# Kernel optimization log

Hardware: AMD Instinct MI355X
Metric: run time of the kernel (lower is better)

The kernel has to match this reference:

```python
import jax, jax.numpy as jnp
import numpy as np

B, S, DIM, H = 2, 2048, 2048, 16
HD = DIM // H  # 128
ROPE_THETA = 10000.0
NEG = -1e9


def setup_inputs() -> dict:
    key = jax.random.key(0)
    ks = jax.random.split(key, 6)
    x = jax.random.normal(ks[0], (B, S, DIM), dtype=jnp.float32)
    # rotary embedding tables: angle[s, j] = s / theta^(2j/HD), j in [0, HD/2)
    inv_freq = 1.0 / (ROPE_THETA ** (jnp.arange(0, HD, 2, dtype=jnp.float32) / HD))
    angles = jnp.arange(S, dtype=jnp.float32)[:, None] * inv_freq[None, :]  # (S, HD/2)
    freqs_cos = jnp.cos(angles)
    freqs_sin = jnp.sin(angles)
    # causal additive mask (1,1,S,S)
    causal = jnp.tril(jnp.ones((S, S), dtype=jnp.bool_))
    mask = jnp.where(causal, 0.0, NEG).astype(jnp.float32)[None, None]
    sc = 1.0 / np.sqrt(DIM)
    wq = jax.random.normal(ks[1], (DIM, DIM), dtype=jnp.float32) * sc
    wk = jax.random.normal(ks[2], (DIM, DIM), dtype=jnp.float32) * sc
    wv = jax.random.normal(ks[3], (DIM, DIM), dtype=jnp.float32) * sc
    wo = jax.random.normal(ks[4], (DIM, DIM), dtype=jnp.float32) * sc
    return {"x": x, "freqs_cos": freqs_cos, "freqs_sin": freqs_sin,
            "mask": mask, "wq": wq, "wk": wk, "wv": wv, "wo": wo}


def _apply_rope(t, cos, sin):
    # t: (B,S,H,HD); cos/sin: (S, HD/2) -> broadcast (1,S,1,HD/2)
    tr = t[..., ::2]
    ti = t[..., 1::2]
    c = cos[None, :, None, :]
    s = sin[None, :, None, :]
    out_r = tr * c - ti * s
    out_i = tr * s + ti * c
    # interleave back: stack on last axis then flatten -> [r0,i0,r1,i1,...]
    return jnp.stack([out_r, out_i], axis=-1).reshape(t.shape)


def reference(x, freqs_cos, freqs_sin, mask, wq, wk, wv, wo):
    b, s, _ = x.shape
    xq = (x @ wq).reshape(b, s, H, HD)
    xk = (x @ wk).reshape(b, s, H, HD)
    xv = (x @ wv).reshape(b, s, H, HD)
    xq = _apply_rope(xq, freqs_cos, freqs_sin)
    xk = _apply_rope(xk, freqs_cos, freqs_sin)
    # (B,H,S,HD)
    q = jnp.transpose(xq, (0, 2, 1, 3)) * (1.0 / np.sqrt(HD))
    k = jnp.transpose(xk, (0, 2, 1, 3))
    v = jnp.transpose(xv, (0, 2, 1, 3))
    attn = jnp.einsum('bhqd,bhkd->bhqk', q, k) + mask[:, :, :s, :s]
    attn = jax.nn.softmax(attn, axis=-1)
    out = jnp.einsum('bhqk,bhkd->bhqd', attn, v)  # (B,H,S,HD)
    out = jnp.transpose(out, (0, 2, 1, 3)).reshape(b, s, H * HD)
    return out @ wo
```

## Files before the change

### kernel.cpp

```cpp
#include <hip/hip_runtime.h>
#include <hip/hip_bf16.h>
#include <cstdint>
#include <cstddef>

#define BB   2
#define SS   2048
#define DD   2048
#define HH   16
#define HDD  128

typedef unsigned short u16;
typedef __attribute__((ext_vector_type(8))) short short8;
typedef __attribute__((ext_vector_type(4))) float f32x4;

__device__ __forceinline__ u16 f2bf(float f) {
  union { float f; uint32_t u; } v; v.f = f;
  uint32_t r = v.u + 0x7fffu + ((v.u >> 16) & 1u);
  return (u16)(r >> 16);
}
__device__ __forceinline__ float bf2f(u16 b) {
  union { uint32_t u; float f; } v; v.u = ((uint32_t)b) << 16;
  return v.f;
}

__device__ __forceinline__ void gload16(const u16* g, u16* l) {
  __builtin_amdgcn_global_load_lds(
      (__attribute__((address_space(1))) void*)g,
      (__attribute__((address_space(3))) void*)l, 16, 0, 0);
}

__global__ void k_cvt(const float* __restrict__ x, u16* __restrict__ o) {
  int i = blockIdx.x * blockDim.x + threadIdx.x;
  const float4 v = reinterpret_cast<const float4*>(x)[i];
  uint2 p;
  p.x = (uint32_t)f2bf(v.x) | ((uint32_t)f2bf(v.y) << 16);
  p.y = (uint32_t)f2bf(v.z) | ((uint32_t)f2bf(v.w) << 16);
  reinterpret_cast<uint2*>(o)[i] = p;
}

__global__ void k_wt(const float* __restrict__ w, u16* __restrict__ wt) {
  __shared__ float t[32][33];
  const int n0 = blockIdx.x * 32, k0 = blockIdx.y * 32;
  const int tx = threadIdx.x, ty = threadIdx.y;
#pragma unroll
  for (int i = 0; i < 32; i += 8)
    t[ty + i][tx] = w[(size_t)(k0 + ty + i) * DD + n0 + tx];
  __syncthreads();
#pragma unroll
  for (int i = 0; i < 32; i += 8)
    wt[(size_t)(n0 + ty + i) * DD + k0 + tx] = f2bf(t[tx][ty + i]);
}

__global__ void k_vt(const u16* __restrict__ V, u16* __restrict__ Vt) {
  __shared__ u16 t[32][33];
  const int s0 = blockIdx.x * 32, d0 = blockIdx.y * 32, bh = blockIdx.z;
  const u16* vb = V + (size_t)bh * SS * HDD;
  u16* vt = Vt + (size_t)bh * SS * HDD;
  const int tx = threadIdx.x, ty = threadIdx.y;
#pragma unroll
  for (int i = 0; i < 32; i += 8)
    t[ty + i][tx] = vb[(size_t)(s0 + ty + i) * HDD + d0 + tx];
  __syncthreads();
#pragma unroll
  for (int i = 0; i < 32; i += 8)
    vt[(size_t)(d0 + ty + i) * SS + s0 + tx] = t[tx][ty + i];
}

__global__ void k_rope(u16* __restrict__ Q, u16* __restrict__ Kb,
                       const float* __restrict__ fc, const float* __restrict__ fs) {
  const int idx = blockIdx.x * blockDim.x + threadIdx.x;
  const int p = idx & 63;
  const int s = (idx >> 6) & (SS - 1);
  const float cv = fc[s * 64 + p], sv = fs[s * 64 + p];
  const size_t off = ((size_t)(idx >> 6)) * HDD + p * 2;
  const float sc = 0.08838834764831845f;
  const float qr = bf2f(Q[off]), qi = bf2f(Q[off + 1]);
  Q[off]      = f2bf((qr * cv - qi * sv) * sc);
  Q[off + 1]  = f2bf((qr * sv + qi * cv) * sc);
  const float kr = bf2f(Kb[off]), ki = bf2f(Kb[off + 1]);
  Kb[off]     = f2bf(kr * cv - ki * sv);
  Kb[off + 1] = f2bf(kr * sv + ki * cv);
}

template <int MODE>
__global__ __launch_bounds__(256) void k_gemm(const u16* __restrict__ A,
                                              const u16* __restrict__ Bt,
                                              void* __restrict__ out) {
  __shared__ __align__(16) u16 As[128 * 32];
  __shared__ __align__(16) u16 Bs[128 * 32];
  const int tid = threadIdx.x;
  const int wave = tid >> 6, lane = tid & 63;
  const int c = lane & 15, g = lane >> 4;
  const int row0 = blockIdx.x * 128, col0 = blockIdx.y * 128;
  const int wm = wave >> 1, wn = wave & 1;
  const int sr = lane >> 2;
  const int sk = (lane & 3) * 8;
  f32x4 acc[4][4] = {};
  for (int k0 = 0; k0 < DD; k0 += 32) {
#pragma unroll
    for (int r = 0; r < 2; ++r) {
      const int chunk = r * 4 + wave;
      const int row = chunk * 16 + sr;
      gload16(A  + (size_t)(row0 + row) * DD + k0 + sk, As + chunk * 512);
      gload16(Bt + (size_t)(col0 + row) * DD + k0 + sk, Bs + chunk * 512);
    }
    __syncthreads();
    short8 a[4], b[4];
#pragma unroll
    for (int i = 0; i < 4; ++i)
      a[i] = *reinterpret_cast<const short8*>(As + (wm * 64 + i * 16 + c) * 32 + g * 8);
#pragma unroll
    for (int j = 0; j < 4; ++j)
      b[j] = *reinterpret_cast<const short8*>(Bs + (wn * 64 + j * 16 + c) * 32 + g * 8);
#pragma unroll
    for (int i = 0; i < 4; ++i)
#pragma unroll
      for (int j = 0; j < 4; ++j)
        acc[i][j] = __builtin_amdgcn_mfma_f32_16x16x32_bf16(a[i], b[j], acc[i][j], 0, 0, 0);
    __syncthreads();
  }
#pragma unroll
  for (int i = 0; i < 4; ++i) {
#pragma unroll
    for (int j = 0; j < 4; ++j) {
      const int mb = row0 + wm * 64 + i * 16 + g * 4;
      const int n  = col0 + wn * 64 + j * 16 + c;
#pragma unroll
      for (int r = 0; r < 4; ++r) {
        const int m = mb + r;
        if (MODE == 0) {
          const int b_ = m >> 11, s_ = m & (SS - 1);
          const int h_ = n >> 7,  d_ = n & (HDD - 1);
          reinterpret_cast<u16*>(out)[(((size_t)(b_ * HH + h_)) * SS + s_) * HDD + d_] =
              f2bf(acc[i][j][r]);
        } else {
          reinterpret_cast<float*>(out)[(size_t)m * DD + n] = acc[i][j][r];
        }
      }
    }
  }
}

__global__ __launch_bounds__(256, 3) void k_attn(const u16* __restrict__ Q,
                                                 const u16* __restrict__ K,
                                                 const u16* __restrict__ Vt,
                                                 u16* __restrict__ O) {
  __shared__ __align__(16) u16 Kt[64 * 128];
  __shared__ __align__(16) u16 Vs[128 * 64];
  __shared__ __align__(16) u16 Pb[4 * 32 * 72];
  const int tid = threadIdx.x;
  const int wave = tid >> 6, lane = tid & 63;
  const int c = lane & 15, g = lane >> 4;
  const int l = blockIdx.x;
  int qi, bh;
  if (l < 256) { qi = 8 + (l & 7); bh = l >> 3; }
  else         { qi = 7 - ((l - 256) & 7); bh = (l - 256) >> 3; }
  const int q0 = qi * 128;
  const u16* Qp = Q  + (size_t)bh * SS * HDD;
  const u16* Kp = K  + (size_t)bh * SS * HDD;
  const u16* Vp = Vt + (size_t)bh * SS * HDD;
  short8 qf[2][4];
#pragma unroll
  for (int ms = 0; ms < 2; ++ms)
#pragma unroll
    for (int kd = 0; kd < 4; ++kd)
      qf[ms][kd] = *reinterpret_cast<const short8*>(
          Qp + (size_t)(q0 + wave * 32 + ms * 16 + c) * HDD + kd * 32 + g * 8);
  f32x4 acc[2][8] = {};
  float psum[2][4] = {};
  const int ntiles = qi * 2 + 2;
  u16* pwav = Pb + wave * (32 * 72);
  const int krl = lane >> 4, kcl = lane & 15;
  const int vrl = lane >> 3, vcl = lane & 7;
  for (int t = 0; t < ntiles; ++t) {
    const int kv0 = t * 64;
#pragma unroll
    for (int j = 0; j < 4; ++j) {
      const int r0k = (j * 4 + wave) * 4;
      const int rowk = r0k + krl;
      gload16(Kp + (size_t)(kv0 + rowk) * HDD + ((kcl ^ (rowk & 15)) << 3),
              Kt + r0k * 128);
      const int r0v = (j * 4 + wave) * 8;
      const int rowv = r0v + vrl;
      gload16(Vp + (size_t)rowv * SS + kv0 + ((vcl ^ (vrl & 7)) << 3),
              Vs + r0v * 64);
    }
    __syncthreads();
    const bool active = kv0 <= q0 + wave * 32 + 31;
    if (active) {
      f32x4 s[2][4] = {};
#pragma unroll
      for (int ns = 0; ns < 4; ++ns) {
#pragma unroll
        for (int kd = 0; kd < 4; ++kd) {
          const short8 b = *reinterpret_cast<const short8*>(
              Kt + (ns * 16 + c) * 128 + (((kd * 4 + g) ^ c) << 3));
          s[0][ns] = __builtin_amdgcn_mfma_f32_16x16x32_bf16(qf[0][kd], b, s[0][ns], 0, 0, 0);
          s[1][ns] = __builtin_amdgcn_mfma_f32_16x16x32_bf16(qf[1][kd], b, s[1][ns], 0, 0, 0);
        }
      }
#pragma unroll
      for (int ms = 0; ms < 2; ++ms) {
        const int qrow = q0 + wave * 32 + ms * 16 + g * 4;
#pragma unroll
        for (int r = 0; r < 4; ++r) {
          u16* pw = pwav + (ms * 16 + g * 4 + r) * 72 + c;
          float rs = 0.f;
#pragma unroll
          for (int ns = 0; ns < 4; ++ns) {
            const bool u = (kv0 + ns * 16 + c) <= (qrow + r);
            const float p = u ? __expf(s[ms][ns][r]) : 0.f;
            rs += p;
            pw[ns * 16] = f2bf(p);
          }
          psum[ms][r] += rs;
        }
      }
      short8 pa[2][2];
#pragma unroll
      for (int ms = 0; ms < 2; ++ms)
#pragma unroll
        for (int kd2 = 0; kd2 < 2; ++kd2)
          pa[ms][kd2] = *reinterpret_cast<const short8*>(
              pwav + (ms * 16 + c) * 72 + kd2 * 32 + g * 8);
#pragma unroll
      for (int nb = 0; nb < 8; ++nb) {
#pragma unroll
        for (int kd2 = 0; kd2 < 2; ++kd2) {
          const short8 vb = *reinterpret_cast<const short8*>(
              Vs + (nb * 16 + c) * 64 + (((kd2 * 4 + g) ^ (c & 7)) << 3));
          acc[0][nb] = __builtin_amdgcn_mfma_f32_16x16x32_bf16(pa[0][kd2], vb, acc[0][nb], 0, 0, 0);
          acc[1][nb] = __builtin_amdgcn_mfma_f32_16x16x32_bf16(pa[1][kd2], vb, acc[1][nb], 0, 0, 0);
        }
      }
    }
    __syncthreads();
  }
  const int b_ = bh >> 4, h_ = bh & 15;
#pragma unroll
  for (int ms = 0; ms < 2; ++ms) {
#pragma unroll
    for (int r = 0; r < 4; ++r) {
      float rs = psum[ms][r];
      rs += __shfl_xor(rs, 1);
      rs += __shfl_xor(rs, 2);
      rs += __shfl_xor(rs, 4);
      rs += __shfl_xor(rs, 8);
      const float inv = 1.f / rs;
      const int s_ = q0 + wave * 32 + ms * 16 + g * 4 + r;
      u16* op = O + ((size_t)(b_ * SS + s_)) * DD + h_ * HDD;
#pragma unroll
      for (int nb = 0; nb < 8; ++nb)
        op[nb * 16 + c] = f2bf(acc[ms][nb][r] * inv);
    }
  }
}

extern "C" void kernel_launch(void* const* d_in, const int* in_sizes, int n_in,
                              void* d_out, int out_size, void* d_ws, size_t ws_size,
                              hipStream_t stream) {
  const float* x  = (const float*)d_in[0];
  const float* fc = (const float*)d_in[1];
  const float* fs = (const float*)d_in[2];
  const float* wq = (const float*)d_in[4];
  const float* wk = (const float*)d_in[5];
  const float* wv = (const float*)d_in[6];
  const float* wo = (const float*)d_in[7];

  u16* ws  = (u16*)d_ws;
  u16* xb  = ws;
  u16* wqt = xb  + 8388608;
  u16* wkt = wqt + 4194304;
  u16* wvt = wkt + 4194304;
  u16* wot = wvt + 4194304;
  u16* Qb  = wot + 4194304;
  u16* Kb  = Qb  + 8388608;
  u16* Vb  = Kb  + 8388608;
  u16* Vtb = Vb  + 8388608;
  u16* ao  = Vtb + 8388608;

  const dim3 tb(32, 8);
  k_cvt<<<8192, 256, 0, stream>>>(x, xb);
  k_wt<<<dim3(64, 64), tb, 0, stream>>>(wq, wqt);
  k_wt<<<dim3(64, 64), tb, 0, stream>>>(wk, wkt);
  k_wt<<<dim3(64, 64), tb, 0, stream>>>(wv, wvt);
  k_wt<<<dim3(64, 64), tb, 0, stream>>>(wo, wot);
  k_gemm<0><<<dim3(32, 16), 256, 0, stream>>>(xb, wqt, (void*)Qb);
  k_gemm<0><<<dim3(32, 16), 256, 0, stream>>>(xb, wkt, (void*)Kb);
  k_gemm<0><<<dim3(32, 16), 256, 0, stream>>>(xb, wvt, (void*)Vb);
  k_rope<<<16384, 256, 0, stream>>>(Qb, Kb, fc, fs);
  k_vt<<<dim3(64, 4, 32), tb, 0, stream>>>(Vb, Vtb);
  k_attn<<<512, 256, 0, stream>>>(Qb, Kb, Vtb, ao);
  k_gemm<1><<<dim3(32, 16), 256, 0, stream>>>(ao, wot, d_out);
}
```

Before: 462.9 us.

## Double-buffer attention K/V tiles and fuse QKV projections into one GEMM launch

The attention kernel now uses 32-wide KV tiles with double-buffered shared memory, so the next tile is prefetched while the current one is computed, and one barrier per tile is removed. The three Q/K/V projection GEMMs are merged into a single launch with a 48-wide grid that writes to contiguous Q/K/V buffers by output column. This relies on wqt/wkt/wvt and Qb/Kb/Vb being adjacent in the workspace. Smaller tiles mean more loop iterations and lower MFMA work per barrier.

```diff
diff --git a/kernel.cpp b/kernel.cpp
--- a/kernel.cpp
+++ b/kernel.cpp
@@ -129,10 +129,11 @@
       for (int r = 0; r < 4; ++r) {
         const int m = mb + r;
         if (MODE == 0) {
+          const int which = n >> 11;
           const int b_ = m >> 11, s_ = m & (SS - 1);
-          const int h_ = n >> 7,  d_ = n & (HDD - 1);
-          reinterpret_cast<u16*>(out)[(((size_t)(b_ * HH + h_)) * SS + s_) * HDD + d_] =
-              f2bf(acc[i][j][r]);
+          const int h_ = (n >> 7) & 15, d_ = n & (HDD - 1);
+          reinterpret_cast<u16*>(out)[(size_t)which * (BB * HH * SS * HDD) +
+              (((size_t)(b_ * HH + h_)) * SS + s_) * HDD + d_] = f2bf(acc[i][j][r]);
         } else {
           reinterpret_cast<float*>(out)[(size_t)m * DD + n] = acc[i][j][r];
         }
@@ -145,9 +146,9 @@
                                                  const u16* __restrict__ K,
                                                  const u16* __restrict__ Vt,
                                                  u16* __restrict__ O) {
-  __shared__ __align__(16) u16 Kt[64 * 128];
-  __shared__ __align__(16) u16 Vs[128 * 64];
-  __shared__ __align__(16) u16 Pb[4 * 32 * 72];
+  __shared__ __align__(16) u16 Kt[2][32 * 128];
+  __shared__ __align__(16) u16 Vs[2][128 * 32];
+  __shared__ __align__(16) u16 Pb[4 * 32 * 40];
   const int tid = threadIdx.x;
   const int wave = tid >> 6, lane = tid & 63;
   const int c = lane & 15, g = lane >> 4;
@@ -168,73 +169,72 @@
           Qp + (size_t)(q0 + wave * 32 + ms * 16 + c) * HDD + kd * 32 + g * 8);
   f32x4 acc[2][8] = {};
   float psum[2][4] = {};
-  const int ntiles = qi * 2 + 2;
-  u16* pwav = Pb + wave * (32 * 72);
+  const int ntiles = (qi + 1) * 4;
+  u16* pwav = Pb + wave * (32 * 40);
   const int krl = lane >> 4, kcl = lane & 15;
-  const int vrl = lane >> 3, vcl = lane & 7;
-  for (int t = 0; t < ntiles; ++t) {
-    const int kv0 = t * 64;
-#pragma unroll
-    for (int j = 0; j < 4; ++j) {
+  const int vrl = lane >> 2, vcl = lane & 3;
+  auto stage = [&](int t) {
+    const int kv0 = t * 32;
+    u16* kb = Kt[t & 1];
+    u16* vb = Vs[t & 1];
+#pragma unroll
+    for (int j = 0; j < 2; ++j) {
       const int r0k = (j * 4 + wave) * 4;
       const int rowk = r0k + krl;
       gload16(Kp + (size_t)(kv0 + rowk) * HDD + ((kcl ^ (rowk & 15)) << 3),
-              Kt + r0k * 128);
-      const int r0v = (j * 4 + wave) * 8;
+              kb + r0k * 128);
+      const int r0v = (j * 4 + wave) * 16;
       const int rowv = r0v + vrl;
-      gload16(Vp + (size_t)rowv * SS + kv0 + ((vcl ^ (vrl & 7)) << 3),
-              Vs + r0v * 64);
-    }
+      gload16(Vp + (size_t)rowv * SS + kv0 + ((vcl ^ (vrl & 3)) << 3),
+              vb + r0v * 32);
+    }
+  };
+  stage(0);
+  for (int t = 0; t < ntiles; ++t) {
     __syncthreads();
+    if (t + 1 < ntiles) stage(t + 1);
+    const int kv0 = t * 32;
     const bool active = kv0 <= q0 + wave * 32 + 31;
-    if (active) {
-      f32x4 s[2][4] = {};
-#pragma unroll
-      for (int ns = 0; ns < 4; ++ns) {
-#pragma unroll
-        for (int kd = 0; kd < 4; ++kd) {
-          const short8 b = *reinterpret_cast<const short8*>(
-              Kt + (ns * 16 + c) * 128 + (((kd * 4 + g) ^ c) << 3));
-          s[0][ns] = __builtin_amdgcn_mfma_f32_16x16x32_bf16(qf[0][kd], b, s[0][ns], 0, 0, 0);
-          s[1][ns] = __builtin_amdgcn_mfma_f32_16x16x32_bf16(qf[1][kd], b, s[1][ns], 0, 0, 0);
+    if (!active) continue;
+    const u16* kb = Kt[t & 1];
+    const u16* vv = Vs[t & 1];
+    f32x4 s[2][2] = {};
+#pragma unroll
+    for (int ns = 0; ns < 2; ++ns)
+#pragma unroll
+      for (int kd = 0; kd < 4; ++kd) {
+        const short8 b = *reinterpret_cast<const short8*>(
+            kb + (ns * 16 + c) * 128 + (((kd * 4 + g) ^ c) << 3));
+        s[0][ns] = __builtin_amdgcn_mfma_f32_16x16x32_bf16(qf[0][kd], b, s[0][ns], 0, 0, 0);
+        s[1][ns] = __builtin_amdgcn_mfma_f32_16x16x32_bf16(qf[1][kd], b, s[1][ns], 0, 0, 0);
+      }
+#pragma unroll
+    for (int ms = 0; ms < 2; ++ms) {
+      const int qrow = q0 + wave * 32 + ms * 16 + g * 4;
+#pragma unroll
+      for (int r = 0; r < 4; ++r) {
+        u16* pw = pwav + (ms * 16 + g * 4 + r) * 40 + c;
+        float rs = 0.f;
+#pragma unroll
+        for (int ns = 0; ns < 2; ++ns) {
+          const bool u = (kv0 + ns * 16 + c) <= (qrow + r);
+          const float p = u ? __expf(s[ms][ns][r]) : 0.f;
+          rs += p;
+          pw[ns * 16] = f2bf(p);
         }
+        psum[ms][r] += rs;
       }
-#pragma unroll
-      for (int ms = 0; ms < 2; ++ms) {
-        const int qrow = q0 + wave * 32 + ms * 16 + g * 4;
-#pragma unroll
-        for (int r = 0; r < 4; ++r) {
-          u16* pw = pwav + (ms * 16 + g * 4 + r) * 72 + c;
-          float rs = 0.f;
-#pragma unroll
-          for (int ns = 0; ns < 4; ++ns) {
-            const bool u = (kv0 + ns * 16 + c) <= (qrow + r);
-            const float p = u ? __expf(s[ms][ns][r]) : 0.f;
-            rs += p;
-            pw[ns * 16] = f2bf(p);
-          }
-          psum[ms][r] += rs;
-        }
-      }
-      short8 pa[2][2];
-#pragma unroll
-      for (int ms = 0; ms < 2; ++ms)
-#pragma unroll
-        for (int kd2 = 0; kd2 < 2; ++kd2)
-          pa[ms][kd2] = *reinterpret_cast<const short8*>(
-              pwav + (ms * 16 + c) * 72 + kd2 * 32 + g * 8);
-#pragma unroll
-      for (int nb = 0; nb < 8; ++nb) {
-#pragma unroll
-        for (int kd2 = 0; kd2 < 2; ++kd2) {
-          const short8 vb = *reinterpret_cast<const short8*>(
-              Vs + (nb * 16 + c) * 64 + (((kd2 * 4 + g) ^ (c & 7)) << 3));
-          acc[0][nb] = __builtin_amdgcn_mfma_f32_16x16x32_bf16(pa[0][kd2], vb, acc[0][nb], 0, 0, 0);
-          acc[1][nb] = __builtin_amdgcn_mfma_f32_16x16x32_bf16(pa[1][kd2], vb, acc[1][nb], 0, 0, 0);
-        }
-      }
-    }
-    __syncthreads();
+    }
+    short8 pa[2];
+    pa[0] = *reinterpret_cast<const short8*>(pwav + c * 40 + g * 8);
+    pa[1] = *reinterpret_cast<const short8*>(pwav + (16 + c) * 40 + g * 8);
+#pragma unroll
+    for (int nb = 0; nb < 8; ++nb) {
+      const short8 vb2 = *reinterpret_cast<const short8*>(
+          vv + (nb * 16 + c) * 32 + ((g ^ (c & 3)) << 3));
+      acc[0][nb] = __builtin_amdgcn_mfma_f32_16x16x32_bf16(pa[0], vb2, acc[0][nb], 0, 0, 0);
+      acc[1][nb] = __builtin_amdgcn_mfma_f32_16x16x32_bf16(pa[1], vb2, acc[1][nb], 0, 0, 0);
+    }
   }
   const int b_ = bh >> 4, h_ = bh & 15;
 #pragma unroll
@@ -285,9 +285,7 @@
   k_wt<<<dim3(64, 64), tb, 0, stream>>>(wk, wkt);
   k_wt<<<dim3(64, 64), tb, 0, stream>>>(wv, wvt);
   k_wt<<<dim3(64, 64), tb, 0, stream>>>(wo, wot);
-  k_gemm<0><<<dim3(32, 16), 256, 0, stream>>>(xb, wqt, (void*)Qb);
-  k_gemm<0><<<dim3(32, 16), 256, 0, stream>>>(xb, wkt, (void*)Kb);
-  k_gemm<0><<<dim3(32, 16), 256, 0, stream>>>(xb, wvt, (void*)Vb);
+  k_gemm<0><<<dim3(32, 48), 256, 0, stream>>>(xb, wqt, (void*)Qb);
   k_rope<<<16384, 256, 0, stream>>>(Qb, Kb, fc, fs);
   k_vt<<<dim3(64, 4, 32), tb, 0, stream>>>(Vb, Vtb);
   k_attn<<<512, 256, 0, stream>>>(Qb, Kb, Vtb, ao);
```

New measurement: 438.2 us. -5.3%, faster.
